# Optimization experiments

Hardware: AMD Instinct MI355X
Metric: run time of the kernel (lower is better)

Reference implementation:

```python
import jax, jax.numpy as jnp
import numpy as np

ALPHA = 1000.0  # Voting(1000) temperature
EPS_NORM = 1e-12
RIDGE = 1e-6


def _edge_index(n):
    # gh(): complete directed graph, edges enumerated i-major, j skipping diagonal.
    ii, jj = np.meshgrid(np.arange(n), np.arange(n), indexing='ij')
    off = ii != jj
    src = ii[off].astype(np.int32)   # G one-hot column = source node
    tgt = jj[off].astype(np.int32)   # H one-hot column = target node
    eid = np.zeros((n, n), dtype=np.int32)
    eid[off] = np.arange(src.size, dtype=np.int32)
    return src, tgt, eid, off


def _l2norm_rows(x):
    return x / jnp.maximum(jnp.linalg.norm(x, axis=1, keepdims=True), EPS_NORM)


def _forward(data1, data2, W, b):
    n1 = data1.shape[0]
    n2 = data2.shape[0]
    src1, tgt1, eid1, off1 = _edge_index(n1)
    src2, tgt2, eid2, off2 = _edge_index(n2)

    # cross-graph embedding update
    Mp0 = data1 @ data2.T                      # [n1, n2]
    m1 = Mp0 @ data2                           # [n1, 512]
    m2 = Mp0.T @ data1                         # [n2, 512]
    lam1 = jax.lax.stop_gradient(
        jnp.linalg.norm(data1, axis=1, keepdims=True)
        / jnp.linalg.norm(m1, axis=1, keepdims=True))
    lam2 = jax.lax.stop_gradient(
        jnp.linalg.norm(data2, axis=1, keepdims=True)
        / jnp.linalg.norm(m2, axis=1, keepdims=True))
    e1 = jax.nn.relu((data1 + lam1 * m1) @ W.T + b)
    e2 = jax.nn.relu((data2 + lam2 * m2) @ W.T + b)
    e1 = _l2norm_rows(e1)
    e2 = _l2norm_rows(e2)

    # edge affinity Me = X2^T Y2 / 2 with X2 = [F@G; F@H] (G/H one-hot => gathers)
    Me = (e1[src1] @ e2[src2].T + e1[tgt1] @ e2[tgt2].T) * 0.5   # [E1, E2]
    Mp = e1 @ e2.T                                               # [n1, n2]

    # Kronecker affinity: M[(i2*n1+i1),(j2*n1+j1)] = Me[eid1[i1,j1], eid2[i2,j2]]
    # (exact value of (a2*K_G) @ K_H^T for complete-graph one-hot incidences)
    g = Me[eid1][:, :, eid2]                                     # [i1, j1, i2, j2]
    mask = off1[:, :, None, None] & off2[None, None, :, :]
    g = jnp.where(mask, g, 0.0)
    Mmat = jnp.transpose(g, (2, 0, 3, 1)).reshape(n1 * n2, n1 * n2)

    Nv = n1 * n2
    kconst = (n1 - 1) * (n2 - 1)
    Q = (kconst + RIDGE) * jnp.eye(Nv, dtype=Mmat.dtype) - Mmat
    Mpp = Mp.T.reshape(Nv)

    # equality constraints of the n1==n2 branch (doubly-stochastic-sum rows),
    # one redundant row dropped so the KKT system is nonsingular
    A1 = jnp.kron(jnp.ones((1, n1), Mmat.dtype), jnp.eye(n2, dtype=Mmat.dtype))
    A2 = jnp.kron(jnp.eye(n1, dtype=Mmat.dtype), jnp.ones((1, n2), Mmat.dtype))
    A = jnp.concatenate([A1, A2], 0)[:-1]
    nc = A.shape[0]

    # QP  min 1/2 z^T Q z - Mpp^T z  s.t. A z = 1  (equality KKT solve;
    # z>=0 handled by the subsequent clamp as in the released pipeline)
    KKT = jnp.block([[Q, A.T], [A, jnp.zeros((nc, nc), Mmat.dtype)]])
    rhs = jnp.concatenate([Mpp, jnp.ones(nc, Mmat.dtype)])
    z = jnp.linalg.solve(KKT, rhs)[:Nv]

    s = z.reshape(n2, n1).T                 # [n1, n2]
    s = jnp.clip(s, 0.0, 1.0)               # relu(s) - relu(s-1)
    s = jax.nn.softmax(ALPHA * s, axis=-1)[None]  # Voting(1000)
    return s


def setup_inputs() -> dict:
    key = jax.random.key(0)
    k1, k2, k3, k4 = jax.random.split(key, 4)
    n, d = 80, 512
    data1 = jax.random.normal(k1, (n, d), dtype=jnp.float32)
    data2 = jax.random.normal(k2, (n, d), dtype=jnp.float32)
    # cross_graph Linear initialized to identity (nn.init.eye_) + tiny jitter
    W = jnp.eye(d, dtype=jnp.float32) + 0.01 * jax.random.normal(k3, (d, d), dtype=jnp.float32)
    b = 0.01 * jax.random.normal(k4, (d,), dtype=jnp.float32)
    return {"data1": data1, "data2": data2, "W": W, "b": b}


def reference(data1, data2, W, b):
    return _forward(data1, data2, W, b)
```

## Files before the change

### kernel.cpp

```cpp
#include <hip/hip_runtime.h>
#include <math.h>

#define N 80
#define D 512
#define NV (N*N)
#define CQ 6241.000001
#define CG_MAX 16

__device__ double g_Mp0[N*N];
__device__ float  g_WT[D*D];
__device__ double g_e[2][N*D];
__device__ double g_P[NV];

__global__ void k_pre(const float* __restrict__ W,
                      const float* __restrict__ d1, const float* __restrict__ d2) {
    int bid = blockIdx.x;
    int tid = threadIdx.x;
    if (bid < 256) {
        __shared__ float t[32][33];
        int c0 = (bid & 15)*32, k0 = (bid >> 4)*32;
        int tx = tid & 31, ty = tid >> 5;
        #pragma unroll
        for (int j = 0; j < 4; ++j) t[ty+8*j][tx] = W[(size_t)(k0+ty+8*j)*D + c0+tx];
        __syncthreads();
        #pragma unroll
        for (int j = 0; j < 4; ++j) g_WT[(size_t)(c0+ty+8*j)*D + k0+tx] = t[tx][ty+8*j];
    } else {
        int gidx = (bid-256)*256 + tid;
        int v = gidx >> 3, ch = gidx & 7;
        int i = v / N, j = v % N;
        const float4* A = reinterpret_cast<const float4*>(d1 + (size_t)i*D);
        const float4* B = reinterpret_cast<const float4*>(d2 + (size_t)j*D);
        double a0=0,a1=0,a2=0,a3=0;
        #pragma unroll
        for (int t = 0; t < 16; ++t) {
            float4 x = A[ch + 8*t], y = B[ch + 8*t];
            a0 += (double)x.x*(double)y.x; a1 += (double)x.y*(double)y.y;
            a2 += (double)x.z*(double)y.z; a3 += (double)x.w*(double)y.w;
        }
        double s = (a0+a1)+(a2+a3);
        #pragma unroll
        for (int o = 1; o < 8; o <<= 1) s += __shfl_xor(s, o, 64);
        if (ch == 0) g_Mp0[i*N+j] = s;
    }
}

__global__ void __launch_bounds__(512,1) k_mue(const float* __restrict__ d1,
                                               const float* __restrict__ d2,
                                               const float* __restrict__ b) {
    __shared__ double mp[N];
    __shared__ double su[D];
    __shared__ double red[512];
    __shared__ double red2[512];
    int bid = blockIdx.x;
    int g = bid / N, row = bid % N;
    int tid = threadIdx.x;
    const float* dsrc = g ? d1 : d2;
    const float* dme  = g ? d2 : d1;

    if (tid < N) mp[tid] = g ? g_Mp0[tid*N + row] : g_Mp0[row*N + tid];
    __syncthreads();

    double m0=0,m1=0,m2=0,m3=0;
    #pragma unroll 4
    for (int j = 0; j < N; j += 4) {
        m0 += mp[j]   * (double)dsrc[(size_t)j*D     + tid];
        m1 += mp[j+1] * (double)dsrc[(size_t)(j+1)*D + tid];
        m2 += mp[j+2] * (double)dsrc[(size_t)(j+2)*D + tid];
        m3 += mp[j+3] * (double)dsrc[(size_t)(j+3)*D + tid];
    }
    double mk = (m0+m1)+(m2+m3);
    double ak = (double)dme[(size_t)row*D + tid];

    red[tid] = ak*ak; red2[tid] = mk*mk; __syncthreads();
    for (int o = 256; o > 0; o >>= 1) {
        if (tid < o) { red[tid] += red[tid+o]; red2[tid] += red2[tid+o]; }
        __syncthreads();
    }
    double lam = sqrt(red[0]) / sqrt(red2[0]);
    __syncthreads();

    su[tid] = ak + lam*mk;
    __syncthreads();

    const float* wt = g_WT + tid;
    double a0=0,a1=0,a2=0,a3=0,a4=0,a5=0,a6=0,a7=0;
    #pragma unroll 8
    for (int t = 0; t < 64; ++t) {
        int c = t*8;
        a0 += su[c+0]*(double)wt[(size_t)(c+0)*D];
        a1 += su[c+1]*(double)wt[(size_t)(c+1)*D];
        a2 += su[c+2]*(double)wt[(size_t)(c+2)*D];
        a3 += su[c+3]*(double)wt[(size_t)(c+3)*D];
        a4 += su[c+4]*(double)wt[(size_t)(c+4)*D];
        a5 += su[c+5]*(double)wt[(size_t)(c+5)*D];
        a6 += su[c+6]*(double)wt[(size_t)(c+6)*D];
        a7 += su[c+7]*(double)wt[(size_t)(c+7)*D];
    }
    double acc = (double)b[tid] + ((a0+a1)+(a2+a3)) + ((a4+a5)+(a6+a7));
    double ek = acc > 0.0 ? acc : 0.0;

    red[tid] = ek*ek; __syncthreads();
    for (int o = 256; o > 0; o >>= 1) { if (tid < o) red[tid] += red[tid+o]; __syncthreads(); }
    double nrm = sqrt(red[0]); if (nrm < 1e-12) nrm = 1e-12;
    g_e[g][(size_t)row*D + tid] = ek / nrm;
}

__global__ void k_p() {
    int gidx = blockIdx.x*256 + threadIdx.x;
    int v = gidx >> 3, ch = gidx & 7;
    int i1 = v % N, i2 = v / N;
    const double2* a = reinterpret_cast<const double2*>(g_e[0] + (size_t)i1*D);
    const double2* c2 = reinterpret_cast<const double2*>(g_e[1] + (size_t)i2*D);
    double a0=0,a1=0;
    #pragma unroll
    for (int t = 0; t < 32; ++t) {
        double2 x = a[ch + 8*t], y = c2[ch + 8*t];
        a0 += x.x*y.x; a1 += x.y*y.y;
    }
    double s = a0+a1;
    #pragma unroll
    for (int o = 1; o < 8; o <<= 1) s += __shfl_xor(s, o, 64);
    if (ch == 0) g_P[v] = s;
}

__device__ __forceinline__ double bredux(double v, double* red4, double* sc, int slot, int tid) {
    #pragma unroll
    for (int o = 32; o > 0; o >>= 1) v += __shfl_down(v, o, 64);
    if ((tid & 63) == 0) red4[tid >> 6] = v;
    __syncthreads();
    if (tid == 0) sc[slot] = red4[0] + red4[1] + red4[2] + red4[3];
    __syncthreads();
    return sc[slot];
}

__global__ void __launch_bounds__(256,1) k_pcgout(float* __restrict__ out) {
    __shared__ double sd[NV];
    __shared__ double sq[NV];
    __shared__ double sRy[N], sCy[N];
    __shared__ double red4[4];
    __shared__ double sc[4];
    const double inv80 = 1.0/80.0, inv6400 = 1.0/6400.0, CHI = 1.0/80.0;
    int tid = threadIdx.x;
    double x[25], r[25], ploc[25];

    #pragma unroll
    for (int j = 0; j < 25; ++j) { int v = tid + 256*j; ploc[j] = g_P[v]; sq[v] = ploc[j]; }
    __syncthreads();

    if (tid < N) {
        double cs = 0.0; const double* dd = sq + tid*N;
        for (int i1 = 0; i1 < N; ++i1) cs += dd[i1];
        sCy[tid] = cs;
    } else if (tid < 2*N) {
        int i1 = tid - N; double rr = 0.0;
        for (int i2 = 0; i2 < N; ++i2) rr += sq[i2*N + i1];
        sRy[i1] = rr;
    }
    __syncthreads();
    if (tid == 0) { double s = 0.0; for (int i = 0; i < N; ++i) s += sCy[i]; sc[0] = s; }
    __syncthreads();
    double Tp = sc[0];
    const double SCALE = 6402.0/160.0;
    double rsp = 0.0;
    #pragma unroll
    for (int j = 0; j < 25; ++j) {
        int v = tid + 256*j; int i1 = v % N, i2 = v / N;
        double rv = SCALE*(ploc[j] - sRy[i1]*inv80 - sCy[i2]*inv80 + Tp*inv6400);
        r[j] = rv; x[j] = 0.0; sd[v] = rv;
        rsp += rv*rv;
    }
    double rs = bredux(rsp, red4, sc, 2, tid);
    double rs0 = rs;

    for (int it = 0; it < CG_MAX && rs > 1e-22*rs0; ++it) {
        #pragma unroll
        for (int j = 0; j < 25; ++j) { int v = tid + 256*j; sq[v] = ploc[j]*sd[v]; }
        __syncthreads();
        if (tid < N) {
            double cs = 0.0; const double* dd = sq + tid*N;
            for (int i1 = 0; i1 < N; ++i1) cs += dd[i1];
            sCy[tid] = cs;
        } else if (tid < 2*N) {
            int i1 = tid - N; double rr = 0.0;
            for (int i2 = 0; i2 < N; ++i2) rr += sq[i2*N + i1];
            sRy[i1] = rr;
        }
        __syncthreads();
        if (tid == 0) { double s = 0.0; for (int i = 0; i < N; ++i) s += sCy[i]; sc[1] = s; }
        __syncthreads();
        double Ty = sc[1];

        double dqp = 0.0;
        #pragma unroll
        for (int j = 0; j < 25; ++j) {
            int v = tid + 256*j; int i1 = v % N, i2 = v / N;
            double qv = CQ*sd[v] - (sq[v] - sRy[i1]*inv80 - sCy[i2]*inv80 + Ty*inv6400);
            sq[v] = qv;
            dqp += sd[v]*qv;
        }
        double dq = bredux(dqp, red4, sc, 3, tid);
        double alpha = rs / dq;

        double rsnp = 0.0;
        #pragma unroll
        for (int j = 0; j < 25; ++j) {
            int v = tid + 256*j;
            x[j] += alpha*sd[v];
            r[j] -= alpha*sq[v];
            rsnp += r[j]*r[j];
        }
        double rsn = bredux(rsnp, red4, sc, 2, tid);
        double beta = rsn / rs;
        rs = rsn;

        #pragma unroll
        for (int j = 0; j < 25; ++j) { int v = tid + 256*j; sd[v] = r[j] + beta*sd[v]; }
        __syncthreads();
    }

    #pragma unroll
    for (int j = 0; j < 25; ++j) {
        int v = tid + 256*j;
        double z = CHI + x[j];
        sq[v] = z < 0.0 ? 0.0 : (z > 1.0 ? 1.0 : z);
    }
    __syncthreads();
    if (tid < N) {
        int i1 = tid;
        double mx = -1e300;
        for (int i2 = 0; i2 < N; ++i2) mx = fmax(mx, sq[i2*N + i1]);
        double s = 0.0;
        for (int i2 = 0; i2 < N; ++i2) {
            double e = exp(1000.0*(sq[i2*N + i1] - mx));
            sd[i2*N + i1] = e; s += e;
        }
        double invs = 1.0 / s;
        for (int i2 = 0; i2 < N; ++i2) out[i1*N + i2] = (float)(sd[i2*N + i1] * invs);
    }
}

extern "C" void kernel_launch(void* const* d_in, const int* in_sizes, int n_in,
                              void* d_out, int out_size, void* d_ws, size_t ws_size,
                              hipStream_t stream) {
    const float* d1 = (const float*)d_in[0];
    const float* d2 = (const float*)d_in[1];
    const float* W  = (const float*)d_in[2];
    const float* b  = (const float*)d_in[3];
    float* out = (float*)d_out;

    k_pre   <<<dim3(456), dim3(256), 0, stream>>>(W, d1, d2);
    k_mue   <<<dim3(160), dim3(512), 0, stream>>>(d1, d2, b);
    k_p     <<<dim3(200), dim3(256), 0, stream>>>();
    k_pcgout<<<dim3(1),   dim3(256), 0, stream>>>(out);
}
```

Measured before the change: 70.13 us.

## Replace PCG solve with fixed four-term Neumann series in final kernel

Replaces the preconditioned conjugate-gradient loop (up to 16 iterations, each with three block-wide reductions) with a fixed four-term Neumann series expansion of the inverse, exploiting that Q is dominated by its large diagonal constant. This removes the dot-product reductions and their barriers from each iteration. The final softmax is also parallelized across all threads instead of 80 threads doing serial strided loops. The risk is reduced accuracy if the truncated series does not converge well enough for the inputs.

```diff
diff --git a/kernel.cpp b/kernel.cpp
--- a/kernel.cpp
+++ b/kernel.cpp
@@ -5,7 +5,7 @@
 #define D 512
 #define NV (N*N)
 #define CQ 6241.000001
-#define CG_MAX 16
+#define NEU_K 4
 
 __device__ double g_Mp0[N*N];
 __device__ float  g_WT[D*D];
@@ -124,98 +124,66 @@
     if (ch == 0) g_P[v] = s;
 }
 
-__device__ __forceinline__ double bredux(double v, double* red4, double* sc, int slot, int tid) {
-    #pragma unroll
-    for (int o = 32; o > 0; o >>= 1) v += __shfl_down(v, o, 64);
-    if ((tid & 63) == 0) red4[tid >> 6] = v;
-    __syncthreads();
-    if (tid == 0) sc[slot] = red4[0] + red4[1] + red4[2] + red4[3];
-    __syncthreads();
-    return sc[slot];
-}
-
-__global__ void __launch_bounds__(256,1) k_pcgout(float* __restrict__ out) {
-    __shared__ double sd[NV];
-    __shared__ double sq[NV];
-    __shared__ double sRy[N], sCy[N];
-    __shared__ double red4[4];
-    __shared__ double sc[4];
+__global__ void __launch_bounds__(256,1) k_out(float* __restrict__ out) {
+    __shared__ double sv[NV];
+    __shared__ double sR[N], sC[N];
+    __shared__ double ssc[4];
     const double inv80 = 1.0/80.0, inv6400 = 1.0/6400.0, CHI = 1.0/80.0;
+    const double invCQ = 1.0/CQ;
     int tid = threadIdx.x;
-    double x[25], r[25], ploc[25];
-
-    #pragma unroll
-    for (int j = 0; j < 25; ++j) { int v = tid + 256*j; ploc[j] = g_P[v]; sq[v] = ploc[j]; }
+    double ploc[25], vv[25], x[25];
+
+    #pragma unroll
+    for (int j = 0; j < 25; ++j) { int v = tid + 256*j; ploc[j] = g_P[v]; sv[v] = ploc[j]; }
     __syncthreads();
 
     if (tid < N) {
-        double cs = 0.0; const double* dd = sq + tid*N;
+        double cs = 0.0; const double* dd = sv + tid*N;
         for (int i1 = 0; i1 < N; ++i1) cs += dd[i1];
-        sCy[tid] = cs;
+        sC[tid] = cs;
     } else if (tid < 2*N) {
         int i1 = tid - N; double rr = 0.0;
-        for (int i2 = 0; i2 < N; ++i2) rr += sq[i2*N + i1];
-        sRy[i1] = rr;
-    }
-    __syncthreads();
-    if (tid == 0) { double s = 0.0; for (int i = 0; i < N; ++i) s += sCy[i]; sc[0] = s; }
-    __syncthreads();
-    double Tp = sc[0];
+        for (int i2 = 0; i2 < N; ++i2) rr += sv[i2*N + i1];
+        sR[i1] = rr;
+    }
+    __syncthreads();
+    if (tid == 0) { double s = 0.0; for (int i = 0; i < N; ++i) s += sC[i]; ssc[0] = s; }
+    __syncthreads();
+    double Tp = ssc[0];
     const double SCALE = 6402.0/160.0;
-    double rsp = 0.0;
     #pragma unroll
     for (int j = 0; j < 25; ++j) {
         int v = tid + 256*j; int i1 = v % N, i2 = v / N;
-        double rv = SCALE*(ploc[j] - sRy[i1]*inv80 - sCy[i2]*inv80 + Tp*inv6400);
-        r[j] = rv; x[j] = 0.0; sd[v] = rv;
-        rsp += rv*rv;
-    }
-    double rs = bredux(rsp, red4, sc, 2, tid);
-    double rs0 = rs;
-
-    for (int it = 0; it < CG_MAX && rs > 1e-22*rs0; ++it) {
-        #pragma unroll
-        for (int j = 0; j < 25; ++j) { int v = tid + 256*j; sq[v] = ploc[j]*sd[v]; }
+        double rv = SCALE*(ploc[j] - sR[i1]*inv80 - sC[i2]*inv80 + Tp*inv6400);
+        vv[j] = rv;
+        x[j]  = rv*invCQ;
+    }
+    __syncthreads();
+
+    for (int k = 0; k < NEU_K; ++k) {
+        #pragma unroll
+        for (int j = 0; j < 25; ++j) { int v = tid + 256*j; sv[v] = ploc[j]*vv[j]; }
         __syncthreads();
         if (tid < N) {
-            double cs = 0.0; const double* dd = sq + tid*N;
+            double cs = 0.0; const double* dd = sv + tid*N;
             for (int i1 = 0; i1 < N; ++i1) cs += dd[i1];
-            sCy[tid] = cs;
+            sC[tid] = cs;
         } else if (tid < 2*N) {
             int i1 = tid - N; double rr = 0.0;
-            for (int i2 = 0; i2 < N; ++i2) rr += sq[i2*N + i1];
-            sRy[i1] = rr;
+            for (int i2 = 0; i2 < N; ++i2) rr += sv[i2*N + i1];
+            sR[i1] = rr;
         }
         __syncthreads();
-        if (tid == 0) { double s = 0.0; for (int i = 0; i < N; ++i) s += sCy[i]; sc[1] = s; }
-        __syncthreads();
-        double Ty = sc[1];
-
-        double dqp = 0.0;
+        if (tid == 0) { double s = 0.0; for (int i = 0; i < N; ++i) s += sC[i]; ssc[1] = s; }
+        __syncthreads();
+        double Ty = ssc[1];
         #pragma unroll
         for (int j = 0; j < 25; ++j) {
             int v = tid + 256*j; int i1 = v % N, i2 = v / N;
-            double qv = CQ*sd[v] - (sq[v] - sRy[i1]*inv80 - sCy[i2]*inv80 + Ty*inv6400);
-            sq[v] = qv;
-            dqp += sd[v]*qv;
+            double mv = ploc[j]*vv[j] - sR[i1]*inv80 - sC[i2]*inv80 + Ty*inv6400;
+            vv[j] = mv*invCQ;
+            x[j] += vv[j]*invCQ;
         }
-        double dq = bredux(dqp, red4, sc, 3, tid);
-        double alpha = rs / dq;
-
-        double rsnp = 0.0;
-        #pragma unroll
-        for (int j = 0; j < 25; ++j) {
-            int v = tid + 256*j;
-            x[j] += alpha*sd[v];
-            r[j] -= alpha*sq[v];
-            rsnp += r[j]*r[j];
-        }
-        double rsn = bredux(rsnp, red4, sc, 2, tid);
-        double beta = rsn / rs;
-        rs = rsn;
-
-        #pragma unroll
-        for (int j = 0; j < 25; ++j) { int v = tid + 256*j; sd[v] = r[j] + beta*sd[v]; }
         __syncthreads();
     }
 
@@ -223,20 +191,31 @@
     for (int j = 0; j < 25; ++j) {
         int v = tid + 256*j;
         double z = CHI + x[j];
-        sq[v] = z < 0.0 ? 0.0 : (z > 1.0 ? 1.0 : z);
+        sv[v] = z < 0.0 ? 0.0 : (z > 1.0 ? 1.0 : z);
     }
     __syncthreads();
     if (tid < N) {
-        int i1 = tid;
         double mx = -1e300;
-        for (int i2 = 0; i2 < N; ++i2) mx = fmax(mx, sq[i2*N + i1]);
+        for (int i2 = 0; i2 < N; ++i2) mx = fmax(mx, sv[i2*N + tid]);
+        sR[tid] = mx;
+    }
+    __syncthreads();
+    #pragma unroll
+    for (int j = 0; j < 25; ++j) {
+        int v = tid + 256*j; int i1 = v % N;
+        sv[v] = exp(1000.0*(sv[v] - sR[i1]));
+    }
+    __syncthreads();
+    if (tid < N) {
         double s = 0.0;
-        for (int i2 = 0; i2 < N; ++i2) {
-            double e = exp(1000.0*(sq[i2*N + i1] - mx));
-            sd[i2*N + i1] = e; s += e;
-        }
-        double invs = 1.0 / s;
-        for (int i2 = 0; i2 < N; ++i2) out[i1*N + i2] = (float)(sd[i2*N + i1] * invs);
+        for (int i2 = 0; i2 < N; ++i2) s += sv[i2*N + tid];
+        sC[tid] = 1.0 / s;
+    }
+    __syncthreads();
+    #pragma unroll
+    for (int j = 0; j < 25; ++j) {
+        int v = tid + 256*j; int i1 = v % N, i2 = v / N;
+        out[i1*N + i2] = (float)(sv[v] * sC[i1]);
     }
 }
 
@@ -249,8 +228,8 @@
     const float* b  = (const float*)d_in[3];
     float* out = (float*)d_out;
 
-    k_pre   <<<dim3(456), dim3(256), 0, stream>>>(W, d1, d2);
-    k_mue   <<<dim3(160), dim3(512), 0, stream>>>(d1, d2, b);
-    k_p     <<<dim3(200), dim3(256), 0, stream>>>();
-    k_pcgout<<<dim3(1),   dim3(256), 0, stream>>>(out);
-}
+    k_pre<<<dim3(456), dim3(256), 0, stream>>>(W, d1, d2);
+    k_mue<<<dim3(160), dim3(512), 0, stream>>>(d1, d2, b);
+    k_p  <<<dim3(200), dim3(256), 0, stream>>>();
+    k_out<<<dim3(1),   dim3(256), 0, stream>>>(out);
+}
```

New measurement: 72.31 us. +3.1%, slower.
